# Optimization experiments

Measured on AMD Instinct MI355X. Metric: run time of the kernel, lower is better.

The kernel has to match this reference:

```python
import jax, jax.numpy as jnp
import numpy as np

N, V, E = 65536, 2048, 1024
TEMPERATURE = 0.5
EPS = 1e-10
LOG_PARAM_Q = -2.995732273553991


def _l2_normalize(x, axis):
    # matches torch F.normalize(p=2): x / max(||x||, 1e-12)
    n = jnp.sqrt(jnp.sum(x * x, axis=axis, keepdims=True))
    return x / jnp.maximum(n, 1e-12)


def setup_inputs() -> dict:
    key = jax.random.key(0)
    k1, k2, k3 = jax.random.split(key, 3)
    z = jax.random.normal(k1, (N, E), dtype=jnp.float32)
    emb_weight = jax.random.normal(k2, (V, E), dtype=jnp.float32)
    U = jax.random.uniform(k3, (N, V), dtype=jnp.float32)
    return {"z": z, "emb_weight": emb_weight, "U": U}


def reference(z, emb_weight, U):
    kappa_q = jnp.exp(jnp.float32(LOG_PARAM_Q)) + jnp.float32(1.0)
    zn = _l2_normalize(z, axis=1)              # [N, E]
    emb = _l2_normalize(emb_weight, axis=1)    # [V, E]
    # logit = -distances = kappa_q * z @ emb.T
    logit = kappa_q * jnp.matmul(zn, emb.T)    # [N, V]
    # gumbel-softmax sample (training branch)
    g = -jnp.log(-jnp.log(U + EPS) + EPS)
    tokens = jax.nn.softmax((logit + g) / TEMPERATURE, axis=-1)  # [N, V]
    z_q = jnp.matmul(tokens, emb)              # [N, E]
    return (tokens, z_q)
```

## Files before the change

kernel.cpp:

```cpp
#include <hip/hip_runtime.h>
#include <hip/hip_bf16.h>
#include <stdint.h>

typedef short bf16x8 __attribute__((ext_vector_type(8)));
typedef float floatx4 __attribute__((ext_vector_type(4)));

#define N_ROWS 65536
#define V_DIM 2048
#define E_DIM 1024

__device__ __forceinline__ short f2bf(float x) {
  union { float f; uint32_t u; } c; c.f = x;
  uint32_t r = (c.u + 0x7FFFu + ((c.u >> 16) & 1u)) >> 16;
  return (short)(uint16_t)r;
}
__device__ __forceinline__ float bf16f(short b) {
  union { uint32_t u; float f; } c; c.u = ((uint32_t)(uint16_t)b) << 16;
  return c.f;
}

__device__ __forceinline__ float wave_sum(float v) {
#pragma unroll
  for (int o = 32; o > 0; o >>= 1) v += __shfl_xor(v, o);
  return v;
}
__device__ __forceinline__ float wave_max(float v) {
#pragma unroll
  for (int o = 32; o > 0; o >>= 1) v = fmaxf(v, __shfl_xor(v, o));
  return v;
}

__device__ __forceinline__ void gll16(const short* g, short* l) {
  __builtin_amdgcn_global_load_lds(
      (const __attribute__((address_space(1))) void*)g,
      (__attribute__((address_space(3))) void*)l, 16, 0, 0);
}

#define FRAG64(base, R, c) \
  (*(const bf16x8*)((const char*)(base) + ((R) << 6) + (((((c) >> 3) ^ ((R) & 3))) << 4)))
#define FRAG(base, R, c) \
  (*(const bf16x8*)((const char*)(base) + ((R) << 7) + (((((c) >> 3) ^ ((R) & 7))) << 4)))

__global__ __launch_bounds__(256) void k_norm_emb(const float* __restrict__ W,
                                                  short* __restrict__ embn,
                                                  short* __restrict__ embnT) {
  const int v = blockIdx.x;
  const int t = threadIdx.x;
  const int w = t >> 6, l = t & 63;
  const float4 val = *(const float4*)&W[(size_t)v * E_DIM + t * 4];
  float ss = val.x * val.x + val.y * val.y + val.z * val.z + val.w * val.w;
  ss = wave_sum(ss);
  __shared__ float red[4];
  if (l == 0) red[w] = ss;
  __syncthreads();
  ss = red[0] + red[1] + red[2] + red[3];
  const float inv = 1.0f / fmaxf(sqrtf(ss), 1e-12f);
  short4 o;
  o.x = f2bf(val.x * inv);
  o.y = f2bf(val.y * inv);
  o.z = f2bf(val.z * inv);
  o.w = f2bf(val.w * inv);
  *(short4*)&embn[(size_t)v * E_DIM + t * 4] = o;
  embnT[(size_t)(t * 4 + 0) * V_DIM + v] = o.x;
  embnT[(size_t)(t * 4 + 1) * V_DIM + v] = o.y;
  embnT[(size_t)(t * 4 + 2) * V_DIM + v] = o.z;
  embnT[(size_t)(t * 4 + 3) * V_DIM + v] = o.w;
}

__global__ __launch_bounds__(256) void k_norm_z(const float* __restrict__ Z,
                                                short* __restrict__ zn) {
  const int w = threadIdx.x >> 6, l = threadIdx.x & 63;
  const int row = blockIdx.x * 4 + w;
  const float* zr = Z + (size_t)row * E_DIM;
  float4 v[4];
  float ss = 0.f;
#pragma unroll
  for (int i = 0; i < 4; ++i) {
    v[i] = *(const float4*)&zr[(i * 64 + l) * 4];
    ss += v[i].x * v[i].x + v[i].y * v[i].y + v[i].z * v[i].z + v[i].w * v[i].w;
  }
  ss = wave_sum(ss);
  const float SCALE = 2.0f * (expf(-2.995732273553991f) + 1.0f);
  const float inv = SCALE / fmaxf(sqrtf(ss), 1e-12f);
  short* zo = zn + (size_t)row * E_DIM;
#pragma unroll
  for (int i = 0; i < 4; ++i) {
    short4 o;
    o.x = f2bf(v[i].x * inv);
    o.y = f2bf(v[i].y * inv);
    o.z = f2bf(v[i].z * inv);
    o.w = f2bf(v[i].w * inv);
    *(short4*)&zo[(i * 64 + l) * 4] = o;
  }
}

template <int KDIM, int NBX, int EPI>
__global__ __launch_bounds__(512, 2) void k_gemm8(
    const short* __restrict__ A, const short* __restrict__ B,
    const float* __restrict__ U, short* __restrict__ Pb,
    float* __restrict__ partials, const float* __restrict__ invsum,
    float* __restrict__ C, int cpx) {
  __shared__ __align__(16) short Sm[65536];
  const int NT = KDIM / 32;
  const int tid = threadIdx.x;
  const int wv = tid >> 6, lane = tid & 63;
  const int lr = lane & 15, lh = lane >> 4;
  const int wr = wv >> 2, wc = wv & 3;
  const int lh8 = lh * 8;
  const int d = blockIdx.x;
  const int L = (d & 7) * cpx + (d >> 3);
  const int by = L / NBX, bx = L % NBX;
  const int m0 = by * 256, n0 = bx * 256;
  const int srow = wv * 16 + (lane >> 2);
  const int sg = (((lane & 3) ^ ((lane >> 2) & 3)) << 3);
  const short* gA = A + (size_t)(m0 + srow) * KDIM + sg;
  const short* gB = B + (size_t)(n0 + srow) * KDIM + sg;

#pragma unroll
  for (int t = 0; t < 2; ++t) {
#pragma unroll
    for (int q = 0; q < 2; ++q) {
      gll16(gA + (size_t)(q * 128) * KDIM + t * 32, Sm + t * 8192 + q * 4096 + wv * 512);
      gll16(gB + (size_t)(q * 128) * KDIM + t * 32, Sm + 32768 + t * 8192 + q * 4096 + wv * 512);
    }
  }
  asm volatile("s_waitcnt vmcnt(4)" ::: "memory");
  __builtin_amdgcn_s_barrier();
  __builtin_amdgcn_sched_barrier(0);

  floatx4 acc[8][4] = {};

#define DO_TILE(KT, STAGE)                                                          \
  {                                                                                 \
    const int cb_ = (KT) & 3;                                                       \
    const short* Ab_ = Sm + cb_ * 8192;                                             \
    const short* Bb_ = Sm + 32768 + cb_ * 8192;                                     \
    short* An_ = Sm + (((KT) + 2) & 3) * 8192;                                      \
    short* Bn_ = Sm + 32768 + (((KT) + 2) & 3) * 8192;                              \
    const size_t kc_ = (size_t)((KT) + 2) * 32;                                     \
    bf16x8 bfr[4];                                                                  \
    _Pragma("unroll")                                                               \
    for (int q = 0; q < 2; ++q) {                                                   \
      if (STAGE) {                                                                  \
        gll16(gA + (size_t)(q * 128) * KDIM + kc_, An_ + q * 4096 + wv * 512);      \
        gll16(gB + (size_t)(q * 128) * KDIM + kc_, Bn_ + q * 4096 + wv * 512);      \
      }                                                                             \
      if (q == 0) {                                                                 \
        _Pragma("unroll")                                                           \
        for (int n = 0; n < 4; ++n) bfr[n] = FRAG64(Bb_, wc * 64 + n * 16 + lr, lh8); \
      }                                                                             \
      bf16x8 af[4];                                                                 \
      const int gm = q * 4;                                                         \
      _Pragma("unroll")                                                             \
      for (int i = 0; i < 4; ++i) af[i] = FRAG64(Ab_, wr * 128 + (gm + i) * 16 + lr, lh8); \
      __builtin_amdgcn_s_setprio(1);                                                \
      _Pragma("unroll")                                                             \
      for (int i = 0; i < 4; ++i) {                                                 \
        _Pragma("unroll")                                                           \
        for (int n = 0; n < 4; ++n)                                                 \
          acc[gm + i][n] =                                                          \
              __builtin_amdgcn_mfma_f32_16x16x32_bf16(af[i], bfr[n], acc[gm + i][n], 0, 0, 0); \
      }                                                                             \
      __builtin_amdgcn_s_setprio(0);                                                \
      if (q == 1) {                                                                 \
        if (STAGE) { asm volatile("s_waitcnt vmcnt(4)" ::: "memory"); }             \
        else      { asm volatile("s_waitcnt vmcnt(0)" ::: "memory"); }              \
      }                                                                             \
      __builtin_amdgcn_s_barrier();                                                 \
      if (q == 1) __builtin_amdgcn_sched_barrier(0);                                \
    }                                                                               \
  }

  for (int kt = 0; kt < NT - 2; ++kt) DO_TILE(kt, 1);
  DO_TILE(NT - 2, 0);
  DO_TILE(NT - 1, 0);
#undef DO_TILE

  const int gr0 = m0 + wr * 128 + lh * 4;
  const int gc0 = n0 + wc * 64 + lr;
  if (EPI == 0) {
    float rs[8][4] = {};
#pragma unroll
    for (int m = 0; m < 8; ++m)
#pragma unroll
      for (int n = 0; n < 4; ++n) {
        const int col = gc0 + n * 16;
#pragma unroll
        for (int j = 0; j < 4; ++j) {
          const int row = gr0 + m * 16 + j;
          const size_t idx = (size_t)row * V_DIM + col;
          const float u = U[idx];
          const float e = __expf(acc[m][n][j] - 2.f * __logf(-__logf(u + 1e-10f) + 1e-10f));
          const short eb = f2bf(e);
          Pb[idx] = eb;
          rs[m][j] += bf16f(eb);
        }
      }
#pragma unroll
    for (int m = 0; m < 8; ++m)
#pragma unroll
      for (int j = 0; j < 4; ++j) {
        float s = rs[m][j];
        s += __shfl_xor(s, 1); s += __shfl_xor(s, 2);
        s += __shfl_xor(s, 4); s += __shfl_xor(s, 8);
        if (lr == 0)
          partials[(size_t)(gr0 + m * 16 + j) * 32 + bx * 4 + wc] = s;
      }
  } else {
#pragma unroll
    for (int m = 0; m < 8; ++m)
#pragma unroll
      for (int j = 0; j < 4; ++j) {
        const int row = gr0 + m * 16 + j;
        const float s = invsum[row];
#pragma unroll
        for (int n = 0; n < 4; ++n)
          C[(size_t)row * E_DIM + gc0 + n * 16] = acc[m][n][j] * s;
      }
  }
}

__global__ __launch_bounds__(256) void k_rowsum_inv(const float* __restrict__ partials,
                                                    float* __restrict__ invsum) {
  const int r = blockIdx.x * 256 + threadIdx.x;
  const float4* p = (const float4*)&partials[(size_t)r * 32];
  float s = 0.f;
#pragma unroll
  for (int i = 0; i < 8; ++i) { float4 v = p[i]; s += v.x + v.y + v.z + v.w; }
  invsum[r] = 1.f / s;
}

__global__ __launch_bounds__(256) void k_token_norm(const short* __restrict__ Pb,
                                                    const float* __restrict__ invsum,
                                                    float* __restrict__ tokens) {
  const size_t stride = (size_t)gridDim.x * 256 * 8;
  for (size_t i = ((size_t)blockIdx.x * 256 + threadIdx.x) * 8;
       i < (size_t)N_ROWS * V_DIM; i += stride) {
    const float s = invsum[i >> 11];
    const bf16x8 v = *(const bf16x8*)&Pb[i];
    float4 o0, o1;
    o0.x = bf16f(v[0]) * s; o0.y = bf16f(v[1]) * s;
    o0.z = bf16f(v[2]) * s; o0.w = bf16f(v[3]) * s;
    o1.x = bf16f(v[4]) * s; o1.y = bf16f(v[5]) * s;
    o1.z = bf16f(v[6]) * s; o1.w = bf16f(v[7]) * s;
    *(float4*)&tokens[i] = o0;
    *(float4*)&tokens[i + 4] = o1;
  }
}

__global__ __launch_bounds__(256) void k_gemm_nt(const short* __restrict__ A,
                                                 const short* __restrict__ B,
                                                 float* __restrict__ C,
                                                 int lda, int ldb, int ldc, int K) {
  __shared__ __align__(16) short As[128][64];
  __shared__ __align__(16) short Bs[128][64];
  const int t = threadIdx.x;
  const int w = t >> 6, l = t & 63;
  const int lr = l & 15, lh = l >> 4;
  const int m0 = blockIdx.y * 128, n0 = blockIdx.x * 128;
  const int wm = (w >> 1) * 64, wn = (w & 1) * 64;
  floatx4 acc[4][4] = {};
  for (int k0 = 0; k0 < K; k0 += 64) {
    __syncthreads();
#pragma unroll
    for (int i = 0; i < 4; ++i) {
      const int c = i * 256 + t;
      const int r = c >> 3, c8 = (c & 7) * 8;
      *(bf16x8*)&As[r][c8] = *(const bf16x8*)&A[(size_t)(m0 + r) * lda + k0 + c8];
      *(bf16x8*)&Bs[r][c8] = *(const bf16x8*)&B[(size_t)(n0 + r) * ldb + k0 + c8];
    }
    __syncthreads();
#pragma unroll
    for (int kk = 0; kk < 64; kk += 32) {
      bf16x8 af[4], bfr[4];
#pragma unroll
      for (int m = 0; m < 4; ++m) af[m] = *(const bf16x8*)&As[wm + m * 16 + lr][kk + lh * 8];
#pragma unroll
      for (int n = 0; n < 4; ++n) bfr[n] = *(const bf16x8*)&Bs[wn + n * 16 + lr][kk + lh * 8];
#pragma unroll
      for (int m = 0; m < 4; ++m)
#pragma unroll
        for (int n = 0; n < 4; ++n)
          acc[m][n] = __builtin_amdgcn_mfma_f32_16x16x32_bf16(af[m], bfr[n], acc[m][n], 0, 0, 0);
    }
  }
#pragma unroll
  for (int m = 0; m < 4; ++m)
#pragma unroll
    for (int n = 0; n < 4; ++n) {
      const int col = n0 + wn + n * 16 + lr;
#pragma unroll
      for (int j = 0; j < 4; ++j)
        C[(size_t)(m0 + wm + m * 16 + lh * 4 + j) * ldc + col] = acc[m][n][j];
    }
}

__global__ __launch_bounds__(256) void k_gemm_nt_f32a(const float* __restrict__ A,
                                                      const short* __restrict__ B,
                                                      float* __restrict__ C,
                                                      int lda, int ldb, int ldc, int K) {
  __shared__ __align__(16) short As[128][64];
  __shared__ __align__(16) short Bs[128][64];
  const int t = threadIdx.x;
  const int w = t >> 6, l = t & 63;
  const int lr = l & 15, lh = l >> 4;
  const int m0 = blockIdx.y * 128, n0 = blockIdx.x * 128;
  const int wm = (w >> 1) * 64, wn = (w & 1) * 64;
  floatx4 acc[4][4] = {};
  for (int k0 = 0; k0 < K; k0 += 64) {
    __syncthreads();
#pragma unroll
    for (int i = 0; i < 4; ++i) {
      const int c = i * 256 + t;
      const int r = c >> 3, c8 = (c & 7) * 8;
      const float4 a0 = *(const float4*)&A[(size_t)(m0 + r) * lda + k0 + c8];
      const float4 a1 = *(const float4*)&A[(size_t)(m0 + r) * lda + k0 + c8 + 4];
      bf16x8 va;
      va[0] = f2bf(a0.x); va[1] = f2bf(a0.y); va[2] = f2bf(a0.z); va[3] = f2bf(a0.w);
      va[4] = f2bf(a1.x); va[5] = f2bf(a1.y); va[6] = f2bf(a1.z); va[7] = f2bf(a1.w);
      *(bf16x8*)&As[r][c8] = va;
      *(bf16x8*)&Bs[r][c8] = *(const bf16x8*)&B[(size_t)(n0 + r) * ldb + k0 + c8];
    }
    __syncthreads();
#pragma unroll
    for (int kk = 0; kk < 64; kk += 32) {
      bf16x8 af[4], bfr[4];
#pragma unroll
      for (int m = 0; m < 4; ++m) af[m] = *(const bf16x8*)&As[wm + m * 16 + lr][kk + lh * 8];
#pragma unroll
      for (int n = 0; n < 4; ++n) bfr[n] = *(const bf16x8*)&Bs[wn + n * 16 + lr][kk + lh * 8];
#pragma unroll
      for (int m = 0; m < 4; ++m)
#pragma unroll
        for (int n = 0; n < 4; ++n)
          acc[m][n] = __builtin_amdgcn_mfma_f32_16x16x32_bf16(af[m], bfr[n], acc[m][n], 0, 0, 0);
    }
  }
#pragma unroll
  for (int m = 0; m < 4; ++m)
#pragma unroll
    for (int n = 0; n < 4; ++n) {
      const int col = n0 + wn + n * 16 + lr;
#pragma unroll
      for (int j = 0; j < 4; ++j)
        C[(size_t)(m0 + wm + m * 16 + lh * 4 + j) * ldc + col] = acc[m][n][j];
    }
}

__global__ __launch_bounds__(256) void k_gumbel_softmax(float* __restrict__ S,
                                                        const float* __restrict__ U) {
  const int t = threadIdx.x;
  const int w = t >> 6, l = t & 63;
  const size_t base = (size_t)blockIdx.x * V_DIM + t * 8;
  const float4 s0 = *(const float4*)&S[base];
  const float4 s1 = *(const float4*)&S[base + 4];
  const float4 u0 = *(const float4*)&U[base];
  const float4 u1 = *(const float4*)&U[base + 4];
  float x[8];
  x[0] = s0.x - 2.f * __logf(-__logf(u0.x + 1e-10f) + 1e-10f);
  x[1] = s0.y - 2.f * __logf(-__logf(u0.y + 1e-10f) + 1e-10f);
  x[2] = s0.z - 2.f * __logf(-__logf(u0.z + 1e-10f) + 1e-10f);
  x[3] = s0.w - 2.f * __logf(-__logf(u0.w + 1e-10f) + 1e-10f);
  x[4] = s1.x - 2.f * __logf(-__logf(u1.x + 1e-10f) + 1e-10f);
  x[5] = s1.y - 2.f * __logf(-__logf(u1.y + 1e-10f) + 1e-10f);
  x[6] = s1.z - 2.f * __logf(-__logf(u1.z + 1e-10f) + 1e-10f);
  x[7] = s1.w - 2.f * __logf(-__logf(u1.w + 1e-10f) + 1e-10f);
  float lm = x[0];
#pragma unroll
  for (int i = 1; i < 8; ++i) lm = fmaxf(lm, x[i]);
  lm = wave_max(lm);
  __shared__ float redA[4], redB[4];
  if (l == 0) redA[w] = lm;
  __syncthreads();
  const float m = fmaxf(fmaxf(redA[0], redA[1]), fmaxf(redA[2], redA[3]));
  float p[8];
  float ls = 0.f;
#pragma unroll
  for (int i = 0; i < 8; ++i) { p[i] = __expf(x[i] - m); ls += p[i]; }
  ls = wave_sum(ls);
  if (l == 0) redB[w] = ls;
  __syncthreads();
  const float inv = 1.0f / (redB[0] + redB[1] + redB[2] + redB[3]);
  float4 o0 = make_float4(p[0] * inv, p[1] * inv, p[2] * inv, p[3] * inv);
  float4 o1 = make_float4(p[4] * inv, p[5] * inv, p[6] * inv, p[7] * inv);
  *(float4*)&S[base] = o0;
  *(float4*)&S[base + 4] = o1;
}

extern "C" void kernel_launch(void* const* d_in, const int* in_sizes, int n_in,
                              void* d_out, int out_size, void* d_ws, size_t ws_size,
                              hipStream_t stream) {
  const float* z = (const float*)d_in[0];
  const float* W = (const float*)d_in[1];
  const float* U = (const float*)d_in[2];
  float* tokens = (float*)d_out;
  float* zq = tokens + (size_t)N_ROWS * V_DIM;
  short* zn = (short*)zq;

  short* embn = (short*)d_ws;
  short* embnT = embn + (size_t)V_DIM * E_DIM;

  const size_t NEED = (size_t)V_DIM * E_DIM * 2 * 2
                    + (size_t)N_ROWS * 32 * 4
                    + (size_t)N_ROWS * 4
                    + (size_t)N_ROWS * V_DIM * 2;

  k_norm_emb<<<V_DIM, 256, 0, stream>>>(W, embn, embnT);
  k_norm_z<<<N_ROWS / 4, 256, 0, stream>>>(z, zn);

  if (ws_size >= NEED) {
    float* partials = (float*)(embnT + (size_t)V_DIM * E_DIM);
    float* invsum = partials + (size_t)N_ROWS * 32;
    short* Pb = (short*)(invsum + N_ROWS);
    k_gemm8<E_DIM, 8, 0><<<2048, 512, 0, stream>>>(
        zn, embn, U, Pb, partials, nullptr, nullptr, 2048 / 8);
    k_rowsum_inv<<<N_ROWS / 256, 256, 0, stream>>>(partials, invsum);
    k_token_norm<<<2048, 256, 0, stream>>>(Pb, invsum, tokens);
    k_gemm8<V_DIM, 4, 1><<<1024, 512, 0, stream>>>(
        Pb, embnT, nullptr, nullptr, nullptr, invsum, zq, 1024 / 8);
  } else {
    k_gemm_nt<<<dim3(V_DIM / 128, N_ROWS / 128), 256, 0, stream>>>(
        zn, embn, tokens, E_DIM, E_DIM, V_DIM, E_DIM);
    k_gumbel_softmax<<<N_ROWS, 256, 0, stream>>>(tokens, U);
    k_gemm_nt_f32a<<<dim3(E_DIM / 128, N_ROWS / 128), 256, 0, stream>>>(
        tokens, embnT, zq, V_DIM, V_DIM, E_DIM, V_DIM);
  }
}
```

Baseline: 1.007 ms.

## Rework LDS swizzle and drop mid-tile barrier in bf16 GEMM main loop

```diff
diff --git a/kernel.cpp b/kernel.cpp
--- a/kernel.cpp
+++ b/kernel.cpp
@@ -36,8 +36,6 @@
       (__attribute__((address_space(3))) void*)l, 16, 0, 0);
 }
 
-#define FRAG64(base, R, c) \
-  (*(const bf16x8*)((const char*)(base) + ((R) << 6) + (((((c) >> 3) ^ ((R) & 3))) << 4)))
 #define FRAG(base, R, c) \
   (*(const bf16x8*)((const char*)(base) + ((R) << 7) + (((((c) >> 3) ^ ((R) & 7))) << 4)))
 
@@ -106,15 +104,17 @@
   const int wv = tid >> 6, lane = tid & 63;
   const int lr = lane & 15, lh = lane >> 4;
   const int wr = wv >> 2, wc = wv & 3;
-  const int lh8 = lh * 8;
   const int d = blockIdx.x;
   const int L = (d & 7) * cpx + (d >> 3);
   const int by = L / NBX, bx = L % NBX;
   const int m0 = by * 256, n0 = bx * 256;
+  const int sg = (((lane & 3) ^ ((lane >> 2) & 3) ^ ((lane >> 4) & 3)) << 3);
   const int srow = wv * 16 + (lane >> 2);
-  const int sg = (((lane & 3) ^ ((lane >> 2) & 3)) << 3);
   const short* gA = A + (size_t)(m0 + srow) * KDIM + sg;
   const short* gB = B + (size_t)(n0 + srow) * KDIM + sg;
+  const int fslot = lh ^ ((lr ^ (lr >> 2)) & 3);
+  const int aoff = wr * 8192 + lr * 64 + fslot * 16;
+  const int boff = wc * 4096 + lr * 64 + fslot * 16;
 
 #pragma unroll
   for (int t = 0; t < 2; ++t) {
@@ -133,42 +133,48 @@
 #define DO_TILE(KT, STAGE)                                                          \
   {                                                                                 \
     const int cb_ = (KT) & 3;                                                       \
-    const short* Ab_ = Sm + cb_ * 8192;                                             \
-    const short* Bb_ = Sm + 32768 + cb_ * 8192;                                     \
+    const char* Ab_ = (const char*)Sm + cb_ * 16384;                                \
+    const char* Bb_ = (const char*)Sm + 65536 + cb_ * 16384;                        \
     short* An_ = Sm + (((KT) + 2) & 3) * 8192;                                      \
     short* Bn_ = Sm + 32768 + (((KT) + 2) & 3) * 8192;                              \
     const size_t kc_ = (size_t)((KT) + 2) * 32;                                     \
-    bf16x8 bfr[4];                                                                  \
+    bf16x8 bfr[4], af[4];                                                           \
     _Pragma("unroll")                                                               \
-    for (int q = 0; q < 2; ++q) {                                                   \
-      if (STAGE) {                                                                  \
+    for (int n = 0; n < 4; ++n) bfr[n] = *(const bf16x8*)(Bb_ + boff + n * 1024);   \
+    _Pragma("unroll")                                                               \
+    for (int i = 0; i < 4; ++i) af[i] = *(const bf16x8*)(Ab_ + aoff + i * 1024);    \
+    if (STAGE) {                                                                    \
+      _Pragma("unroll")                                                             \
+      for (int q = 0; q < 2; ++q) {                                                 \
         gll16(gA + (size_t)(q * 128) * KDIM + kc_, An_ + q * 4096 + wv * 512);      \
         gll16(gB + (size_t)(q * 128) * KDIM + kc_, Bn_ + q * 4096 + wv * 512);      \
       }                                                                             \
-      if (q == 0) {                                                                 \
-        _Pragma("unroll")                                                           \
-        for (int n = 0; n < 4; ++n) bfr[n] = FRAG64(Bb_, wc * 64 + n * 16 + lr, lh8); \
-      }                                                                             \
-      bf16x8 af[4];                                                                 \
-      const int gm = q * 4;                                                         \
+    }                                                                               \
+    __builtin_amdgcn_s_setprio(1);                                                  \
+    _Pragma("unroll")                                                               \
+    for (int i = 0; i < 4; ++i) {                                                   \
       _Pragma("unroll")                                                             \
-      for (int i = 0; i < 4; ++i) af[i] = FRAG64(Ab_, wr * 128 + (gm + i) * 16 + lr, lh8); \
-      __builtin_amdgcn_s_setprio(1);                                                \
+      for (int n = 0; n < 4; ++n)                                                   \
+        acc[i][n] =                                                                 \
+            __builtin_amdgcn_mfma_f32_16x16x32_bf16(af[i], bfr[n], acc[i][n], 0, 0, 0); \
+    }                                                                               \
+    __builtin_amdgcn_s_setprio(0);                                                  \
+    _Pragma("unroll")                                                               \
+    for (int i = 0; i < 4; ++i)                                                     \
+      af[i] = *(const bf16x8*)(Ab_ + aoff + 4096 + i * 1024);                       \
+    __builtin_amdgcn_s_setprio(1);                                                  \
+    _Pragma("unroll")                                                               \
+    for (int i = 0; i < 4; ++i) {                                                   \
       _Pragma("unroll")                                                             \
-      for (int i = 0; i < 4; ++i) {                                                 \
-        _Pragma("unroll")                                                           \
-        for (int n = 0; n < 4; ++n)                                                 \
-          acc[gm + i][n] =                                                          \
-              __builtin_amdgcn_mfma_f32_16x16x32_bf16(af[i], bfr[n], acc[gm + i][n], 0, 0, 0); \
-      }                                                                             \
-      __builtin_amdgcn_s_setprio(0);                                                \
-      if (q == 1) {                                                                 \
-        if (STAGE) { asm volatile("s_waitcnt vmcnt(4)" ::: "memory"); }             \
-        else      { asm volatile("s_waitcnt vmcnt(0)" ::: "memory"); }              \
-      }                                                                             \
-      __builtin_amdgcn_s_barrier();                                                 \
-      if (q == 1) __builtin_amdgcn_sched_barrier(0);                                \
+      for (int n = 0; n < 4; ++n)                                                   \
+        acc[4 + i][n] =                                                             \
+            __builtin_amdgcn_mfma_f32_16x16x32_bf16(af[i], bfr[n], acc[4 + i][n], 0, 0, 0); \
     }                                                                               \
+    __builtin_amdgcn_s_setprio(0);                                                  \
+    if (STAGE) { asm volatile("s_waitcnt vmcnt(4)" ::: "memory"); }                 \
+    else       { asm volatile("s_waitcnt vmcnt(0)" ::: "memory"); }                 \
+    __builtin_amdgcn_s_barrier();                                                   \
+    __builtin_amdgcn_sched_barrier(0);                                              \
   }
 
   for (int kt = 0; kt < NT - 2; ++kt) DO_TILE(kt, 1);
```

Result: no change. 1.004 ms (-0.2%).
